# Optimization experiments

Hardware: AMD Instinct MI355X
Metric: run time of the kernel (lower is better)

Reference implementation:

```python
import jax, jax.numpy as jnp
import numpy as np

EMBED_DIM = 512
N_HEADS = 8
HEAD_DIM = EMBED_DIM // N_HEADS
MAX_GENES = 5000
SPARSITY_RATIO = 0.1
WINDOW = 20  # SparseAttention local window


def make_sparse_mask(key):
    # local band |i-j| <= window//2, plus random connections, plus diagonal
    idx = jnp.arange(MAX_GENES)
    mask = jnp.abs(idx[:, None] - idx[None, :]) <= (WINDOW // 2)
    n_random = int(SPARSITY_RATIO * MAX_GENES * MAX_GENES)
    k1, k2 = jax.random.split(key)
    ri = jax.random.randint(k1, (n_random,), 0, MAX_GENES)
    rj = jax.random.randint(k2, (n_random,), 0, MAX_GENES)
    mask = mask.at[ri, rj].set(True)
    mask = mask.at[idx, idx].set(True)
    return mask  # bool [MAX_GENES, MAX_GENES]


def setup_inputs() -> dict:
    key = jax.random.key(0)
    ks = jax.random.split(key, 10)
    B, S, E = 1, 4096, EMBED_DIM
    x = jax.random.normal(ks[0], (B, S, E), dtype=jnp.float32)
    init = lambda k: jax.random.normal(k, (E, E), dtype=jnp.float32) * 0.02
    return {
        "x": x,
        "Wq": init(ks[1]), "bq": jnp.zeros((E,), jnp.float32),
        "Wk": init(ks[2]), "bk": jnp.zeros((E,), jnp.float32),
        "Wv": init(ks[3]), "bv": jnp.zeros((E,), jnp.float32),
        "Wo": init(ks[4]), "bo": jnp.zeros((E,), jnp.float32),
        "mask": make_sparse_mask(ks[5]),
    }


def reference(x, Wq, bq, Wk, bk, Wv, bv, Wo, bo, mask):
    B, S, E = x.shape
    H, D = N_HEADS, HEAD_DIM
    # QKV projections (torch Linear: x @ W.T + b), split heads -> [B,H,S,D]
    Q = (x @ Wq.T + bq).reshape(B, S, H, D).transpose(0, 2, 1, 3)
    K = (x @ Wk.T + bk).reshape(B, S, H, D).transpose(0, 2, 1, 3)
    V = (x @ Wv.T + bv).reshape(B, S, H, D).transpose(0, 2, 1, 3)
    scale = 1.0 / jnp.sqrt(jnp.asarray(D, dtype=jnp.float32))
    scores = jnp.einsum('bhsd,bhtd->bhst', Q, K) * scale
    m = mask[:S, :S]  # static sparse pattern
    # original: scores*mask then masked_fill(mask==0, -inf) -> equivalent where
    scores = jnp.where(m[None, None], scores, -jnp.inf)
    w = jax.nn.softmax(scores, axis=-1)
    w = jnp.nan_to_num(w, nan=0.0)  # diag is always unmasked, but keep faithful
    out = jnp.einsum('bhst,bhtd->bhsd', w, V)
    out = out.transpose(0, 2, 1, 3).reshape(B, S, E)
    return out @ Wo.T + bo
```

## Files before the change

kernel.cpp:

```cpp
#include <hip/hip_runtime.h>
#include <hip/hip_bf16.h>
#include <stdint.h>

#define S 4096
#define E 512
#define H 8
#define D 64
#define MROW 5000

typedef __hip_bfloat16 bf16;
typedef __attribute__((ext_vector_type(8))) short bf16x8;
typedef __attribute__((ext_vector_type(4))) float f32x4;

#define CMUL (0.125f * 1.4426950408889634f)

__global__ __launch_bounds__(256) void prep(
    const void* __restrict__ mask, unsigned long long* __restrict__ bitsT,
    const float* __restrict__ x,  const float* __restrict__ wq,
    const float* __restrict__ wk, const float* __restrict__ wv,
    const float* __restrict__ wo, const float* __restrict__ bq,
    const float* __restrict__ bk, const float* __restrict__ bv,
    const float* __restrict__ bo,
    bf16* __restrict__ xb, bf16* __restrict__ wcat, bf16* __restrict__ wob,
    bf16* __restrict__ bcat, bf16* __restrict__ bob)
{
    const int tid = threadIdx.x;
    const int b   = blockIdx.x;
    {
        const float* srcs[9] = {x, wq, wk, wv, wo, bq, bk, bv, bo};
        bf16* dsts[9] = {xb, wcat, wcat + 262144, wcat + 524288, wob,
                         bcat, bcat + 512, bcat + 1024, bob};
        const int cnts[9] = {2097152, 262144, 262144, 262144, 262144,
                             512, 512, 512, 512};
        const int ngroups = (2097152 + 4 * 262144 + 4 * 512) / 4;
        for (int g = b * 256 + tid; g < ngroups; g += 2048 * 256) {
            int e = g * 4;
            int seg = 0;
            while (e >= cnts[seg]) { e -= cnts[seg]; ++seg; }
            float4 v = *(const float4*)(srcs[seg] + e);
            union { bf16 h[4]; uint2 u; } cv;
            cv.h[0] = (bf16)v.x; cv.h[1] = (bf16)v.y;
            cv.h[2] = (bf16)v.z; cv.h[3] = (bf16)v.w;
            *(uint2*)(dsts[seg] + e) = cv.u;
        }
    }
    {
        const unsigned int* mw32 = (const unsigned int*)mask;
        int lane = tid & 63;
        int hit = 0;
#pragma unroll
        for (int i = 0; i < 8; ++i) {
            unsigned int w = mw32[lane + i * 64];
            if (w > 1u && (w & 0xFEFEFEFEu) == 0u) hit = 1;
        }
        const bool isbyte = (__ballot(hit) != 0ull);
        int wid  = (b * 256 + tid) >> 6;
        int nwav = (2048 * 256) >> 6;
        int total = (S / 64) * S;
        for (int w = wid; w < total; w += nwav) {
            int word = w >> 12;
            int row  = w & (S - 1);
            int col  = word * 64 + lane;
            unsigned int v;
            if (isbyte) v = ((const unsigned char*)mask)[(size_t)row * MROW + col];
            else        v = ((const unsigned int*)mask)[(size_t)row * MROW + col];
            unsigned long long bb = __ballot(v != 0u);
            if (lane == 0) bitsT[(size_t)word * S + row] = bb;
        }
    }
}

__global__ __launch_bounds__(256) void gemm_qkv(const bf16* __restrict__ A,
                                                const bf16* __restrict__ W,
                                                const bf16* __restrict__ bias,
                                                bf16* __restrict__ out)
{
    __shared__ bf16 As[64][72];
    __shared__ bf16 Bs[64][72];
    const int tid  = threadIdx.x;
    const int wid  = tid >> 6, lane = tid & 63;
    const int quad = lane >> 4, l15 = lane & 15;
    const int nbase = blockIdx.x * 64;
    const int mbase = blockIdx.y * 64;
    const int m0 = wid * 16;

    f32x4 acc[4];
#pragma unroll
    for (int i = 0; i < 4; ++i) acc[i] = (f32x4){0.f, 0.f, 0.f, 0.f};

    for (int kt = 0; kt < E / 64; ++kt) {
        const int kb = kt * 64;
        __syncthreads();
#pragma unroll
        for (int i = 0; i < 2; ++i) {
            int slot = tid + i * 256;
            int row = slot >> 3, kg = slot & 7;
            *(uint4*)&As[row][kg * 8] = *(const uint4*)&A[(size_t)(mbase + row) * E + kb + kg * 8];
            *(uint4*)&Bs[row][kg * 8] = *(const uint4*)&W[(size_t)(nbase + row) * E + kb + kg * 8];
        }
        __syncthreads();
        bf16x8 a0 = *(bf16x8*)&As[m0 + l15][quad * 8];
        bf16x8 a1 = *(bf16x8*)&As[m0 + l15][32 + quad * 8];
#pragma unroll
        for (int nt = 0; nt < 4; ++nt) {
            bf16x8 b0 = *(bf16x8*)&Bs[nt * 16 + l15][quad * 8];
            bf16x8 b1 = *(bf16x8*)&Bs[nt * 16 + l15][32 + quad * 8];
            acc[nt] = __builtin_amdgcn_mfma_f32_16x16x32_bf16(a0, b0, acc[nt], 0, 0, 0);
            acc[nt] = __builtin_amdgcn_mfma_f32_16x16x32_bf16(a1, b1, acc[nt], 0, 0, 0);
        }
    }
#pragma unroll
    for (int nt = 0; nt < 4; ++nt) {
        int col = nbase + nt * 16 + l15;
        float bv = (float)bias[col];
#pragma unroll
        for (int r = 0; r < 4; ++r) {
            int row = mbase + m0 + quad * 4 + r;
            float v = acc[nt][r] + bv;
            int t = col >> 9, hh = (col >> 6) & 7, d = col & 63;
            if (t == 0) v *= CMUL;
            out[((size_t)t * H + hh) * S * D + (size_t)row * D + d] = (bf16)v;
        }
    }
}

__global__ __launch_bounds__(256) void attn(const bf16* __restrict__ Qp,
                                            const bf16* __restrict__ Kp,
                                            const bf16* __restrict__ Vp,
                                            const unsigned long long* __restrict__ bitsT,
                                            float* __restrict__ Opart,
                                            float* __restrict__ Lpart,
                                            int ktper)
{
    __shared__ __align__(16) char smem[25600];
    bf16 (*Ps)[16][72] = (bf16(*)[16][72])smem;
    bf16 (*Ks)[64]     = (bf16(*)[64])(smem + 9216);
    bf16 (*Vts)[64]    = (bf16(*)[64])(smem + 17408);

    const int tid  = threadIdx.x;
    const int wid  = tid >> 6, lane = tid & 63;
    const int quad = lane >> 4, l15 = lane & 15;
    const int qt = blockIdx.x, h = blockIdx.y, split = blockIdx.z;
    const int qbase = qt * 64;
    const int m0 = wid * 16;
    const bf16* Qh = Qp + (size_t)h * S * D;
    const bf16* Kh = Kp + (size_t)h * S * D;
    const bf16* Vh = Vp + (size_t)h * S * D;

    const int krow0 = tid >> 3, kkg = tid & 7;
    const int krow1 = (tid + 256) >> 3;
    const int ksw0 = (kkg ^ (krow0 & 7)) * 8;
    const int ksw1 = (kkg ^ (krow1 & 7)) * 8;
    const int vt0 = (tid & 31) * 2, vd0 = (tid >> 5) * 8;

    const bf16* qrow = Qh + (size_t)(qbase + m0 + l15) * D;
    bf16x8 aq0 = *(const bf16x8*)(qrow + quad * 8);
    bf16x8 aq1 = *(const bf16x8*)(qrow + 32 + quad * 8);

    bf16x8 bl;
    {
        union { short s; bf16 b; } one; one.b = (bf16)1.0f;
        short v = (l15 == 0) ? one.s : (short)0;
#pragma unroll
        for (int j = 0; j < 8; ++j) bl[j] = v;
    }

    f32x4 o[4];
#pragma unroll
    for (int dt = 0; dt < 4; ++dt) o[dt] = (f32x4){0.f, 0.f, 0.f, 0.f};
    f32x4 accl = (f32x4){0.f, 0.f, 0.f, 0.f};

    const int kt0 = split * ktper, kt1 = kt0 + ktper;

    uint4 kq0, kq1, vq0, vq1;
    {
        const int kbase = kt0 * 64;
        kq0 = *(const uint4*)&Kh[(size_t)(kbase + krow0) * D + kkg * 8];
        kq1 = *(const uint4*)&Kh[(size_t)(kbase + krow1) * D + kkg * 8];
        vq0 = *(const uint4*)&Vh[(size_t)(kbase + vt0) * D + vd0];
        vq1 = *(const uint4*)&Vh[(size_t)(kbase + vt0 + 1) * D + vd0];
    }

    const unsigned long long* mb = bitsT + (size_t)kt0 * S + qbase + m0 + l15;

    const int ksw_rd = (l15 & 7);
#pragma unroll 1
    for (int kt = kt0; kt < kt1; ++kt) {
        __syncthreads();
        *(uint4*)&Ks[krow0][ksw0] = kq0;
        *(uint4*)&Ks[krow1][ksw1] = kq1;
        {
            const unsigned int* w0 = (const unsigned int*)&vq0;
            const unsigned int* w1 = (const unsigned int*)&vq1;
#pragma unroll
            for (int j = 0; j < 8; ++j) {
                unsigned int pk = __builtin_amdgcn_perm(
                    w1[j >> 1], w0[j >> 1],
                    (j & 1) ? 0x07060302u : 0x05040100u);
                *(unsigned int*)&Vts[vd0 + j][vt0 ^ (j * 8)] = pk;
            }
        }
        if (kt + 1 < kt1) {
            const int kb2 = (kt + 1) * 64;
            kq0 = *(const uint4*)&Kh[(size_t)(kb2 + krow0) * D + kkg * 8];
            kq1 = *(const uint4*)&Kh[(size_t)(kb2 + krow1) * D + kkg * 8];
            vq0 = *(const uint4*)&Vh[(size_t)(kb2 + vt0) * D + vd0];
            vq1 = *(const uint4*)&Vh[(size_t)(kb2 + vt0 + 1) * D + vd0];
        }
        unsigned long long mw = *mb;
        mb += S;
        __syncthreads();

        f32x4 sc[4];
        {
            f32x4 z = (f32x4){0.f, 0.f, 0.f, 0.f};
#pragma unroll
            for (int nt = 0; nt < 4; ++nt) {
                bf16x8 kb0 = *(bf16x8*)&Ks[nt * 16 + l15][(quad ^ ksw_rd) * 8];
                bf16x8 kb1 = *(bf16x8*)&Ks[nt * 16 + l15][((quad + 4) ^ ksw_rd) * 8];
                sc[nt] = __builtin_amdgcn_mfma_f32_16x16x32_bf16(kb0, aq0, z, 0, 0, 0);
                sc[nt] = __builtin_amdgcn_mfma_f32_16x16x32_bf16(kb1, aq1, sc[nt], 0, 0, 0);
            }
        }
        const unsigned long long sh = mw >> (quad * 4);
        const unsigned int wlo = (unsigned int)sh;
        const unsigned int whi = (unsigned int)(sh >> 32);
#pragma unroll
        for (int nt = 0; nt < 4; ++nt) {
            const unsigned int wsel = (nt < 2) ? wlo : whi;
            unsigned int a[4];
#pragma unroll
            for (int r = 0; r < 4; ++r) {
                const int bit = (nt & 1) * 16 + r;
                float s = ((wsel >> bit) & 1u) ? sc[nt][r] : -200.0f;
                a[r] = __float_as_uint(__builtin_amdgcn_exp2f(s)) + 0x8000u;
            }
            uint2 pk;
            pk.x = __builtin_amdgcn_perm(a[1], a[0], 0x07060302u);
            pk.y = __builtin_amdgcn_perm(a[3], a[2], 0x07060302u);
            *(uint2*)&Ps[wid][l15][nt * 16 + quad * 4] = pk;
        }
        bf16x8 ap0 = *(bf16x8*)&Ps[wid][l15][quad * 8];
        bf16x8 ap1 = *(bf16x8*)&Ps[wid][l15][32 + quad * 8];
        accl = __builtin_amdgcn_mfma_f32_16x16x32_bf16(ap0, bl, accl, 0, 0, 0);
        accl = __builtin_amdgcn_mfma_f32_16x16x32_bf16(ap1, bl, accl, 0, 0, 0);
#pragma unroll
        for (int dt = 0; dt < 4; ++dt) {
            bf16x8 bv0 = *(bf16x8*)&Vts[dt * 16 + l15][(quad ^ ksw_rd) * 8];
            bf16x8 bv1 = *(bf16x8*)&Vts[dt * 16 + l15][((quad + 4) ^ ksw_rd) * 8];
            o[dt] = __builtin_amdgcn_mfma_f32_16x16x32_bf16(ap0, bv0, o[dt], 0, 0, 0);
            o[dt] = __builtin_amdgcn_mfma_f32_16x16x32_bf16(ap1, bv1, o[dt], 0, 0, 0);
        }
    }
    float* Op = Opart + (size_t)(split * H + h) * S * D;
    float* Lp = Lpart + (size_t)(split * H + h) * S;
#pragma unroll
    for (int r = 0; r < 4; ++r) {
        int row = qbase + m0 + quad * 4 + r;
        if (l15 == 0) Lp[row] = accl[r];
#pragma unroll
        for (int dt = 0; dt < 4; ++dt)
            Op[(size_t)row * D + dt * 16 + l15] = o[dt][r];
    }
}

__global__ __launch_bounds__(256) void gemm_out(const float* __restrict__ Opart,
                                                const float* __restrict__ Lpart,
                                                const bf16* __restrict__ W,
                                                const bf16* __restrict__ bias,
                                                float* __restrict__ out, int nsplit)
{
    __shared__ bf16 As[64][72];
    __shared__ bf16 Bs[64][72];
    const int tid  = threadIdx.x;
    const int wid  = tid >> 6, lane = tid & 63;
    const int quad = lane >> 4, l15 = lane & 15;
    const int nbase = blockIdx.x * 64;
    const int mbase = blockIdx.y * 64;
    const int m0 = wid * 16;
    const size_t oh = (size_t)H * S * D;

    f32x4 acc[4];
#pragma unroll
    for (int i = 0; i < 4; ++i) acc[i] = (f32x4){0.f, 0.f, 0.f, 0.f};

    for (int kt = 0; kt < E / 64; ++kt) {
        const int kb = kt * 64;
        const int h = kt;
        __syncthreads();
#pragma unroll
        for (int i = 0; i < 2; ++i) {
            int slot = tid + i * 256;
            int row = slot >> 3, kg = slot & 7;
            int qrow = mbase + row;
            size_t base = ((size_t)h * S + qrow) * D + kg * 8;
            float a[8] = {0, 0, 0, 0, 0, 0, 0, 0};
            float l = 0.f;
            for (int s = 0; s < nsplit; ++s) {
                float4 p0 = *(const float4*)(Opart + (size_t)s * oh + base);
                float4 p1 = *(const float4*)(Opart + (size_t)s * oh + base + 4);
                a[0] += p0.x; a[1] += p0.y; a[2] += p0.z; a[3] += p0.w;
                a[4] += p1.x; a[5] += p1.y; a[6] += p1.z; a[7] += p1.w;
                l += Lpart[(size_t)s * H * S + (size_t)h * S + qrow];
            }
            float inv = (l > 0.f) ? 1.f / l : 0.f;
            union { bf16 hh[8]; uint4 u; } cv;
#pragma unroll
            for (int j = 0; j < 8; ++j) cv.hh[j] = (bf16)(a[j] * inv);
            *(uint4*)&As[row][kg * 8] = cv.u;
            *(uint4*)&Bs[row][kg * 8] = *(const uint4*)&W[(size_t)(nbase + row) * E + kb + kg * 8];
        }
        __syncthreads();
        bf16x8 a0 = *(bf16x8*)&As[m0 + l15][quad * 8];
        bf16x8 a1 = *(bf16x8*)&As[m0 + l15][32 + quad * 8];
#pragma unroll
        for (int nt = 0; nt < 4; ++nt) {
            bf16x8 b0 = *(bf16x8*)&Bs[nt * 16 + l15][quad * 8];
            bf16x8 b1 = *(bf16x8*)&Bs[nt * 16 + l15][32 + quad * 8];
            acc[nt] = __builtin_amdgcn_mfma_f32_16x16x32_bf16(a0, b0, acc[nt], 0, 0, 0);
            acc[nt] = __builtin_amdgcn_mfma_f32_16x16x32_bf16(a1, b1, acc[nt], 0, 0, 0);
        }
    }
#pragma unroll
    for (int nt = 0; nt < 4; ++nt) {
        int col = nbase + nt * 16 + l15;
        float bv = (float)bias[col];
#pragma unroll
        for (int r = 0; r < 4; ++r) {
            int row = mbase + m0 + quad * 4 + r;
            out[(size_t)row * E + col] = acc[nt][r] + bv;
        }
    }
}

extern "C" void kernel_launch(void* const* d_in, const int* in_sizes, int n_in,
                              void* d_out, int out_size, void* d_ws, size_t ws_size,
                              hipStream_t stream)
{
    char* ws = (char*)d_ws;
    const size_t MB = (size_t)1 << 20;
    bf16* Qw   = (bf16*)(ws + 0 * MB);
    bf16* Kw   = (bf16*)(ws + 4 * MB);
    bf16* Vw   = (bf16*)(ws + 8 * MB);
    unsigned long long* bitsT = (unsigned long long*)(ws + 16 * MB);
    bf16* xb   = (bf16*)(ws + 18 * MB);
    bf16* Wcat = (bf16*)(ws + 22 * MB);
    bf16* Wob  = (bf16*)(ws + 24 * MB);
    bf16* bcat = (bf16*)(ws + 25 * MB);
    bf16* bob  = (bf16*)(ws + 25 * MB + 8192);
    float* Opart = (float*)(ws + 26 * MB);

    int nsplit = (ws_size >= 59 * MB) ? 4 : 2;
    int ktper  = (S / 64) / nsplit;
    float* Lpart = (float*)(ws + 26 * MB + (size_t)nsplit * 8 * MB);

    hipLaunchKernelGGL(prep, dim3(2048), dim3(256), 0, stream,
                       d_in[9], bitsT,
                       (const float*)d_in[0], (const float*)d_in[1],
                       (const float*)d_in[3], (const float*)d_in[5],
                       (const float*)d_in[7], (const float*)d_in[2],
                       (const float*)d_in[4], (const float*)d_in[6],
                       (const float*)d_in[8],
                       xb, Wcat, Wob, bcat, bob);
    hipLaunchKernelGGL(gemm_qkv, dim3(24, 64), dim3(256), 0, stream,
                       xb, Wcat, bcat, Qw);
    hipLaunchKernelGGL(attn, dim3(S / 64, H, nsplit), dim3(256), 0, stream,
                       Qw, Kw, Vw, bitsT, Opart, Lpart, ktper);
    hipLaunchKernelGGL(gemm_out, dim3(8, 64), dim3(256), 0, stream,
                       Opart, Lpart, Wob, bob, (float*)d_out, nsplit);
}
```

Before: 301.7 us.

## Process 32 query rows per wave in attention and split out combine kernel

The attention kernel now gives each wave 32 query rows instead of 16, doubling the query tile per block to 128. Each K/V tile loaded into shared memory is therefore reused for twice as many queries, halving K/V traffic and the synchronisation count per query. The split-reduction and normalisation move out of gemm_out into a separate combine kernel that writes a bf16 activation buffer, so gemm_out no longer redoes the split-sum for each of its 8 column blocks. This costs more registers and shared memory per block, half as many attention blocks, and one extra launch plus an intermediate buffer round trip.

Result: faster. 269.7 us (-10.6%).

```diff
diff --git a/kernel.cpp b/kernel.cpp
--- a/kernel.cpp
+++ b/kernel.cpp
@@ -132,17 +132,17 @@
                                             float* __restrict__ Lpart,
                                             int ktper)
 {
-    __shared__ __align__(16) char smem[25600];
-    bf16 (*Ps)[16][72] = (bf16(*)[16][72])smem;
-    bf16 (*Ks)[64]     = (bf16(*)[64])(smem + 9216);
-    bf16 (*Vts)[64]    = (bf16(*)[64])(smem + 17408);
+    __shared__ __align__(16) char smem[34816];
+    bf16 (*Ps)[32][72] = (bf16(*)[32][72])smem;
+    bf16 (*Ks)[64]     = (bf16(*)[64])(smem + 18432);
+    bf16 (*Vts)[64]    = (bf16(*)[64])(smem + 26624);
 
     const int tid  = threadIdx.x;
     const int wid  = tid >> 6, lane = tid & 63;
     const int quad = lane >> 4, l15 = lane & 15;
-    const int qt = blockIdx.x, h = blockIdx.y, split = blockIdx.z;
-    const int qbase = qt * 64;
-    const int m0 = wid * 16;
+    const int qb = blockIdx.x, h = blockIdx.y, split = blockIdx.z;
+    const int qbase = qb * 128;
+    const int m0 = wid * 32;
     const bf16* Qh = Qp + (size_t)h * S * D;
     const bf16* Kh = Kp + (size_t)h * S * D;
     const bf16* Vh = Vp + (size_t)h * S * D;
@@ -153,9 +153,11 @@
     const int ksw1 = (kkg ^ (krow1 & 7)) * 8;
     const int vt0 = (tid & 31) * 2, vd0 = (tid >> 5) * 8;
 
-    const bf16* qrow = Qh + (size_t)(qbase + m0 + l15) * D;
-    bf16x8 aq0 = *(const bf16x8*)(qrow + quad * 8);
-    bf16x8 aq1 = *(const bf16x8*)(qrow + 32 + quad * 8);
+    const bf16* qr0 = Qh + (size_t)(qbase + m0 + l15) * D;
+    bf16x8 aq00 = *(const bf16x8*)(qr0 + quad * 8);
+    bf16x8 aq01 = *(const bf16x8*)(qr0 + 32 + quad * 8);
+    bf16x8 aq10 = *(const bf16x8*)(qr0 + 16 * D + quad * 8);
+    bf16x8 aq11 = *(const bf16x8*)(qr0 + 16 * D + 32 + quad * 8);
 
     bf16x8 bl;
     {
@@ -165,10 +167,14 @@
         for (int j = 0; j < 8; ++j) bl[j] = v;
     }
 
-    f32x4 o[4];
-#pragma unroll
-    for (int dt = 0; dt < 4; ++dt) o[dt] = (f32x4){0.f, 0.f, 0.f, 0.f};
-    f32x4 accl = (f32x4){0.f, 0.f, 0.f, 0.f};
+    f32x4 o[4][2];
+#pragma unroll
+    for (int dt = 0; dt < 4; ++dt)
+#pragma unroll
+        for (int u = 0; u < 2; ++u) o[dt][u] = (f32x4){0.f, 0.f, 0.f, 0.f};
+    f32x4 accl[2];
+    accl[0] = (f32x4){0.f, 0.f, 0.f, 0.f};
+    accl[1] = (f32x4){0.f, 0.f, 0.f, 0.f};
 
     const int kt0 = split * ktper, kt1 = kt0 + ktper;
 
@@ -181,7 +187,8 @@
         vq1 = *(const uint4*)&Vh[(size_t)(kbase + vt0 + 1) * D + vd0];
     }
 
-    const unsigned long long* mb = bitsT + (size_t)kt0 * S + qbase + m0 + l15;
+    const unsigned long long* mb0 = bitsT + (size_t)kt0 * S + qbase + m0 + l15;
+    const unsigned long long* mb1 = mb0 + 16;
 
     const int ksw_rd = (l15 & 7);
 #pragma unroll 1
@@ -207,68 +214,107 @@
             vq0 = *(const uint4*)&Vh[(size_t)(kb2 + vt0) * D + vd0];
             vq1 = *(const uint4*)&Vh[(size_t)(kb2 + vt0 + 1) * D + vd0];
         }
-        unsigned long long mw = *mb;
-        mb += S;
-        __syncthreads();
-
-        f32x4 sc[4];
+        unsigned long long mw0 = *mb0; mb0 += S;
+        unsigned long long mw1 = *mb1; mb1 += S;
+        __syncthreads();
+
+        f32x4 sc[2][4];
         {
             f32x4 z = (f32x4){0.f, 0.f, 0.f, 0.f};
 #pragma unroll
             for (int nt = 0; nt < 4; ++nt) {
                 bf16x8 kb0 = *(bf16x8*)&Ks[nt * 16 + l15][(quad ^ ksw_rd) * 8];
                 bf16x8 kb1 = *(bf16x8*)&Ks[nt * 16 + l15][((quad + 4) ^ ksw_rd) * 8];
-                sc[nt] = __builtin_amdgcn_mfma_f32_16x16x32_bf16(kb0, aq0, z, 0, 0, 0);
-                sc[nt] = __builtin_amdgcn_mfma_f32_16x16x32_bf16(kb1, aq1, sc[nt], 0, 0, 0);
+                sc[0][nt] = __builtin_amdgcn_mfma_f32_16x16x32_bf16(kb0, aq00, z, 0, 0, 0);
+                sc[0][nt] = __builtin_amdgcn_mfma_f32_16x16x32_bf16(kb1, aq01, sc[0][nt], 0, 0, 0);
+                sc[1][nt] = __builtin_amdgcn_mfma_f32_16x16x32_bf16(kb0, aq10, z, 0, 0, 0);
+                sc[1][nt] = __builtin_amdgcn_mfma_f32_16x16x32_bf16(kb1, aq11, sc[1][nt], 0, 0, 0);
             }
         }
-        const unsigned long long sh = mw >> (quad * 4);
-        const unsigned int wlo = (unsigned int)sh;
-        const unsigned int whi = (unsigned int)(sh >> 32);
-#pragma unroll
-        for (int nt = 0; nt < 4; ++nt) {
-            const unsigned int wsel = (nt < 2) ? wlo : whi;
-            unsigned int a[4];
-#pragma unroll
-            for (int r = 0; r < 4; ++r) {
-                const int bit = (nt & 1) * 16 + r;
-                float s = ((wsel >> bit) & 1u) ? sc[nt][r] : -200.0f;
-                a[r] = __float_as_uint(__builtin_amdgcn_exp2f(s)) + 0x8000u;
+#pragma unroll
+        for (int u = 0; u < 2; ++u) {
+            const unsigned long long sh = (u ? mw1 : mw0) >> (quad * 4);
+            const unsigned int wlo = (unsigned int)sh;
+            const unsigned int whi = (unsigned int)(sh >> 32);
+#pragma unroll
+            for (int nt = 0; nt < 4; ++nt) {
+                const unsigned int wsel = (nt < 2) ? wlo : whi;
+                unsigned int a[4];
+#pragma unroll
+                for (int r = 0; r < 4; ++r) {
+                    const int bit = (nt & 1) * 16 + r;
+                    float s = ((wsel >> bit) & 1u) ? sc[u][nt][r] : -200.0f;
+                    a[r] = __float_as_uint(__builtin_amdgcn_exp2f(s)) + 0x8000u;
+                }
+                uint2 pk;
+                pk.x = __builtin_amdgcn_perm(a[1], a[0], 0x07060302u);
+                pk.y = __builtin_amdgcn_perm(a[3], a[2], 0x07060302u);
+                *(uint2*)&Ps[wid][u * 16 + l15][nt * 16 + quad * 4] = pk;
             }
-            uint2 pk;
-            pk.x = __builtin_amdgcn_perm(a[1], a[0], 0x07060302u);
-            pk.y = __builtin_amdgcn_perm(a[3], a[2], 0x07060302u);
-            *(uint2*)&Ps[wid][l15][nt * 16 + quad * 4] = pk;
-        }
-        bf16x8 ap0 = *(bf16x8*)&Ps[wid][l15][quad * 8];
-        bf16x8 ap1 = *(bf16x8*)&Ps[wid][l15][32 + quad * 8];
-        accl = __builtin_amdgcn_mfma_f32_16x16x32_bf16(ap0, bl, accl, 0, 0, 0);
-        accl = __builtin_amdgcn_mfma_f32_16x16x32_bf16(ap1, bl, accl, 0, 0, 0);
+        }
+        bf16x8 ap00 = *(bf16x8*)&Ps[wid][l15][quad * 8];
+        bf16x8 ap01 = *(bf16x8*)&Ps[wid][l15][32 + quad * 8];
+        bf16x8 ap10 = *(bf16x8*)&Ps[wid][16 + l15][quad * 8];
+        bf16x8 ap11 = *(bf16x8*)&Ps[wid][16 + l15][32 + quad * 8];
+        accl[0] = __builtin_amdgcn_mfma_f32_16x16x32_bf16(ap00, bl, accl[0], 0, 0, 0);
+        accl[0] = __builtin_amdgcn_mfma_f32_16x16x32_bf16(ap01, bl, accl[0], 0, 0, 0);
+        accl[1] = __builtin_amdgcn_mfma_f32_16x16x32_bf16(ap10, bl, accl[1], 0, 0, 0);
+        accl[1] = __builtin_amdgcn_mfma_f32_16x16x32_bf16(ap11, bl, accl[1], 0, 0, 0);
 #pragma unroll
         for (int dt = 0; dt < 4; ++dt) {
             bf16x8 bv0 = *(bf16x8*)&Vts[dt * 16 + l15][(quad ^ ksw_rd) * 8];
             bf16x8 bv1 = *(bf16x8*)&Vts[dt * 16 + l15][((quad + 4) ^ ksw_rd) * 8];
-            o[dt] = __builtin_amdgcn_mfma_f32_16x16x32_bf16(ap0, bv0, o[dt], 0, 0, 0);
-            o[dt] = __builtin_amdgcn_mfma_f32_16x16x32_bf16(ap1, bv1, o[dt], 0, 0, 0);
+            o[dt][0] = __builtin_amdgcn_mfma_f32_16x16x32_bf16(ap00, bv0, o[dt][0], 0, 0, 0);
+            o[dt][0] = __builtin_amdgcn_mfma_f32_16x16x32_bf16(ap01, bv1, o[dt][0], 0, 0, 0);
+            o[dt][1] = __builtin_amdgcn_mfma_f32_16x16x32_bf16(ap10, bv0, o[dt][1], 0, 0, 0);
+            o[dt][1] = __builtin_amdgcn_mfma_f32_16x16x32_bf16(ap11, bv1, o[dt][1], 0, 0, 0);
         }
     }
     float* Op = Opart + (size_t)(split * H + h) * S * D;
     float* Lp = Lpart + (size_t)(split * H + h) * S;
 #pragma unroll
-    for (int r = 0; r < 4; ++r) {
-        int row = qbase + m0 + quad * 4 + r;
-        if (l15 == 0) Lp[row] = accl[r];
-#pragma unroll
-        for (int dt = 0; dt < 4; ++dt)
-            Op[(size_t)row * D + dt * 16 + l15] = o[dt][r];
-    }
-}
-
-__global__ __launch_bounds__(256) void gemm_out(const float* __restrict__ Opart,
-                                                const float* __restrict__ Lpart,
+    for (int u = 0; u < 2; ++u)
+#pragma unroll
+        for (int r = 0; r < 4; ++r) {
+            int row = qbase + m0 + u * 16 + quad * 4 + r;
+            if (l15 == 0) Lp[row] = accl[u][r];
+#pragma unroll
+            for (int dt = 0; dt < 4; ++dt)
+                Op[(size_t)row * D + dt * 16 + l15] = o[dt][u][r];
+        }
+}
+
+__global__ __launch_bounds__(256) void combine(const float* __restrict__ Opart,
+                                               const float* __restrict__ Lpart,
+                                               bf16* __restrict__ Ab, int nsplit)
+{
+    const size_t oh = (size_t)H * S * D;
+    int g = blockIdx.x * 256 + threadIdx.x;
+    int row = g >> 6;
+    int cg  = g & 63;
+    int hh  = cg >> 3;
+    int d0  = (cg & 7) * 8;
+    size_t base = ((size_t)hh * S + row) * D + d0;
+    float a[8] = {0.f, 0.f, 0.f, 0.f, 0.f, 0.f, 0.f, 0.f};
+    float l = 0.f;
+    for (int s = 0; s < nsplit; ++s) {
+        float4 p0 = *(const float4*)(Opart + (size_t)s * oh + base);
+        float4 p1 = *(const float4*)(Opart + (size_t)s * oh + base + 4);
+        a[0] += p0.x; a[1] += p0.y; a[2] += p0.z; a[3] += p0.w;
+        a[4] += p1.x; a[5] += p1.y; a[6] += p1.z; a[7] += p1.w;
+        l += Lpart[(size_t)s * H * S + (size_t)hh * S + row];
+    }
+    float inv = (l > 0.f) ? 1.f / l : 0.f;
+    union { bf16 hb[8]; uint4 u; } cv;
+#pragma unroll
+    for (int j = 0; j < 8; ++j) cv.hb[j] = (bf16)(a[j] * inv);
+    *(uint4*)&Ab[(size_t)row * E + hh * 64 + d0] = cv.u;
+}
+
+__global__ __launch_bounds__(256) void gemm_out(const bf16* __restrict__ A,
                                                 const bf16* __restrict__ W,
                                                 const bf16* __restrict__ bias,
-                                                float* __restrict__ out, int nsplit)
+                                                float* __restrict__ out)
 {
     __shared__ bf16 As[64][72];
     __shared__ bf16 Bs[64][72];
@@ -278,7 +324,6 @@
     const int nbase = blockIdx.x * 64;
     const int mbase = blockIdx.y * 64;
     const int m0 = wid * 16;
-    const size_t oh = (size_t)H * S * D;
 
     f32x4 acc[4];
 #pragma unroll
@@ -286,28 +331,12 @@
 
     for (int kt = 0; kt < E / 64; ++kt) {
         const int kb = kt * 64;
-        const int h = kt;
         __syncthreads();
 #pragma unroll
         for (int i = 0; i < 2; ++i) {
             int slot = tid + i * 256;
             int row = slot >> 3, kg = slot & 7;
-            int qrow = mbase + row;
-            size_t base = ((size_t)h * S + qrow) * D + kg * 8;
-            float a[8] = {0, 0, 0, 0, 0, 0, 0, 0};
-            float l = 0.f;
-            for (int s = 0; s < nsplit; ++s) {
-                float4 p0 = *(const float4*)(Opart + (size_t)s * oh + base);
-                float4 p1 = *(const float4*)(Opart + (size_t)s * oh + base + 4);
-                a[0] += p0.x; a[1] += p0.y; a[2] += p0.z; a[3] += p0.w;
-                a[4] += p1.x; a[5] += p1.y; a[6] += p1.z; a[7] += p1.w;
-                l += Lpart[(size_t)s * H * S + (size_t)h * S + qrow];
-            }
-            float inv = (l > 0.f) ? 1.f / l : 0.f;
-            union { bf16 hh[8]; uint4 u; } cv;
-#pragma unroll
-            for (int j = 0; j < 8; ++j) cv.hh[j] = (bf16)(a[j] * inv);
-            *(uint4*)&As[row][kg * 8] = cv.u;
+            *(uint4*)&As[row][kg * 8] = *(const uint4*)&A[(size_t)(mbase + row) * E + kb + kg * 8];
             *(uint4*)&Bs[row][kg * 8] = *(const uint4*)&W[(size_t)(nbase + row) * E + kb + kg * 8];
         }
         __syncthreads();
@@ -342,6 +371,7 @@
     bf16* Qw   = (bf16*)(ws + 0 * MB);
     bf16* Kw   = (bf16*)(ws + 4 * MB);
     bf16* Vw   = (bf16*)(ws + 8 * MB);
+    bf16* Ab   = (bf16*)(ws + 12 * MB);
     unsigned long long* bitsT = (unsigned long long*)(ws + 16 * MB);
     bf16* xb   = (bf16*)(ws + 18 * MB);
     bf16* Wcat = (bf16*)(ws + 22 * MB);
@@ -364,8 +394,10 @@
                        xb, Wcat, Wob, bcat, bob);
     hipLaunchKernelGGL(gemm_qkv, dim3(24, 64), dim3(256), 0, stream,
                        xb, Wcat, bcat, Qw);
-    hipLaunchKernelGGL(attn, dim3(S / 64, H, nsplit), dim3(256), 0, stream,
+    hipLaunchKernelGGL(attn, dim3(S / 128, H, nsplit), dim3(256), 0, stream,
                        Qw, Kw, Vw, bitsT, Opart, Lpart, ktper);
+    hipLaunchKernelGGL(combine, dim3(1024), dim3(256), 0, stream,
+                       Opart, Lpart, Ab, nsplit);
     hipLaunchKernelGGL(gemm_out, dim3(8, 64), dim3(256), 0, stream,
-                       Opart, Lpart, Wob, bob, (float*)d_out, nsplit);
-}
+                       Ab, Wob, bob, (float*)d_out);
+}
```
